# Optimization experiments

Hardware: AMD Instinct MI355X
Metric: run time of the kernel (lower is better)

Reference implementation:

```python
import jax, jax.numpy as jnp
import numpy as np
import math

# dims
B, T, HFEAT, E = 32, 8, 128, 128
NUM_CLS, NUM_GLOBAL = 4, 2
NSP = NUM_CLS + NUM_GLOBAL            # 6 special tokens
SCALES = (1, 4, 8)
WINDOW = 4
NHEAD = 8
DH = E // NHEAD                        # 16
NLAYERS = 2                            # blocks per scale = ceil(6/3)
NS = len(SCALES)
F = 512                                # dim_feedforward
ROPE_BASE = 100000.0
NEG = -1e9


def setup_inputs() -> dict:
    key = jax.random.key(0)
    ks = jax.random.split(key, 16)
    def rn(k, shape, s=0.02):
        return jax.random.normal(k, shape, jnp.float32) * s
    inp = {
        'embeddings': jax.random.normal(ks[0], (B, T, NSP + HFEAT, E), jnp.float32),
        'cls_tokens': rn(ks[1], (NUM_CLS, E)),
        'global_tokens': rn(ks[2], (NUM_GLOBAL, E)),
        'Wq': rn(ks[3], (NS, NLAYERS, E, E)),
        'bq': jnp.zeros((NS, NLAYERS, E), jnp.float32),
        'Wk': rn(ks[4], (NS, NLAYERS, E, E)),
        'bk': jnp.zeros((NS, NLAYERS, E), jnp.float32),
        'Wv': rn(ks[5], (NS, NLAYERS, E, E)),
        'bv': jnp.zeros((NS, NLAYERS, E), jnp.float32),
        'Wo': rn(ks[6], (NS, NLAYERS, E, E)),
        'bo': jnp.zeros((NS, NLAYERS, E), jnp.float32),
        'ln1_g': jnp.ones((NS, NLAYERS, E), jnp.float32),
        'ln1_b': jnp.zeros((NS, NLAYERS, E), jnp.float32),
        'ln2_g': jnp.ones((NS, NLAYERS, E), jnp.float32),
        'ln2_b': jnp.zeros((NS, NLAYERS, E), jnp.float32),
        'W1': rn(ks[7], (NS, NLAYERS, E, F)),
        'b1': jnp.zeros((NS, NLAYERS, F), jnp.float32),
        'W2': rn(ks[8], (NS, NLAYERS, F, E)),
        'b2': jnp.zeros((NS, NLAYERS, E), jnp.float32),
        'out_g': jnp.ones((E,), jnp.float32),
        'out_b': jnp.zeros((E,), jnp.float32),
    }
    return inp


def _layernorm(x, g, b, eps=1e-5):
    mu = x.mean(-1, keepdims=True)
    var = ((x - mu) ** 2).mean(-1, keepdims=True)
    return (x - mu) * jax.lax.rsqrt(var + eps) * g + b


def _rope(x):
    # x: (BT, L, H, DH); rotate-half RoPE over head dim
    L = x.shape[1]
    half = DH // 2
    inv = ROPE_BASE ** (-jnp.arange(half, dtype=jnp.float32) / half)
    ang = jnp.arange(L, dtype=jnp.float32)[:, None] * inv[None, :]   # (L, half)
    cos = jnp.cos(ang)[None, :, None, :]
    sin = jnp.sin(ang)[None, :, None, :]
    x1, x2 = x[..., :half], x[..., half:]
    return jnp.concatenate([x1 * cos - x2 * sin, x1 * sin + x2 * cos], axis=-1)


def _sparse_bias(L):
    # global(first NSP) rows/cols fully connected, others window +-WINDOW, diag allowed
    i = jnp.arange(L)
    allowed = (jnp.abs(i[:, None] - i[None, :]) <= WINDOW) | (i[:, None] < NSP) | (i[None, :] < NSP)
    return jnp.where(allowed, 0.0, NEG).astype(jnp.float32)  # (L, L) additive


def _encoder(x, s, Wq, bq, Wk, bk, Wv, bv, Wo, bo, ln1_g, ln1_b, ln2_g, ln2_b, W1, b1, W2, b2, bias):
    # x: (BT, L, E); pre-norm transformer encoder with RoPE attention
    BT, L, _ = x.shape
    for l in range(NLAYERS):
        h = _layernorm(x, ln1_g[s, l], ln1_b[s, l])
        q = (h @ Wq[s, l] + bq[s, l]).reshape(BT, L, NHEAD, DH)
        k = (h @ Wk[s, l] + bk[s, l]).reshape(BT, L, NHEAD, DH)
        v = (h @ Wv[s, l] + bv[s, l]).reshape(BT, L, NHEAD, DH)
        q, k = _rope(q), _rope(k)
        scores = jnp.einsum('blhd,bmhd->bhlm', q, k) / math.sqrt(DH) + bias[None, None]
        attn = jax.nn.softmax(scores, axis=-1)
        o = jnp.einsum('bhlm,bmhd->blhd', attn, v).reshape(BT, L, E)
        x = x + o @ Wo[s, l] + bo[s, l]
        h2 = _layernorm(x, ln2_g[s, l], ln2_b[s, l])
        x = x + jax.nn.gelu(h2 @ W1[s, l] + b1[s, l]) @ W2[s, l] + b2[s, l]
    return x


def reference(embeddings, cls_tokens, global_tokens, Wq, bq, Wk, bk, Wv, bv, Wo, bo,
              ln1_g, ln1_b, ln2_g, ln2_b, W1, b1, W2, b2, out_g, out_b):
    Bb, Tt, HC, Ee = embeddings.shape
    feats = embeddings[..., NSP:, :]                                 # (B,T,H,E)
    specials = jnp.broadcast_to(
        jnp.concatenate([cls_tokens, global_tokens], axis=0)[None, None],
        (Bb, Tt, NSP, Ee))
    cls_per_scale = []
    for s, g in enumerate(SCALES):
        H = feats.shape[2]
        K = H // g  # H divisible by all scales
        grouped = feats.reshape(Bb, Tt, K, g, Ee).mean(axis=3)       # contiguous mean grouping
        seq = jnp.concatenate([specials, grouped], axis=2)           # (B,T,L,E)
        L = NSP + K
        x = seq.reshape(Bb * Tt, L, Ee)
        bias = _sparse_bias(L)
        out = _encoder(x, s, Wq, bq, Wk, bk, Wv, bv, Wo, bo,
                       ln1_g, ln1_b, ln2_g, ln2_b, W1, b1, W2, b2, bias)
        cls_per_scale.append(out.reshape(Bb, Tt, L, Ee)[..., :NUM_CLS, :])
    cls_out = jnp.stack(cls_per_scale, axis=0).mean(axis=0)          # (B,T,num_cls,E)
    cls_out = _layernorm(cls_out, out_g, out_b)
    return cls_out.reshape(Bb, Tt, NUM_CLS * Ee)
```

## Files before the change

### kernel.cpp

```cpp
#include <hip/hip_runtime.h>
#include <hip/hip_bf16.h>

#define BT     256
#define EDIM   128
#define NSP    6
#define RT     49664
#define O1     34304
#define O2     44032
#define KSTR   20

typedef unsigned short u16;
typedef short s16x8 __attribute__((ext_vector_type(8)));
typedef float f32x4 __attribute__((ext_vector_type(4)));

__device__ __forceinline__ float u2f(u16 u){ union{unsigned i; float f;} v; v.i=((unsigned)u)<<16; return v.f; }
__device__ __forceinline__ u16 f2u(float f){
  union{float f; unsigned i;} v; v.f = f;
  unsigned r = v.i + 0x7FFF + ((v.i >> 16) & 1);
  return (u16)(r >> 16);
}
__device__ __forceinline__ float ldin(const void* p, size_t idx, int flag){
  return flag ? u2f(((const u16*)p)[idx]) : ((const float*)p)[idx];
}
__device__ __forceinline__ void unp8(uint4 v, float* f){
  f[0]=u2f((u16)(v.x)); f[1]=u2f((u16)(v.x>>16));
  f[2]=u2f((u16)(v.y)); f[3]=u2f((u16)(v.y>>16));
  f[4]=u2f((u16)(v.z)); f[5]=u2f((u16)(v.z>>16));
  f[6]=u2f((u16)(v.w)); f[7]=u2f((u16)(v.w>>16));
}

__device__ __forceinline__ void rowinfo(int row, int& s, int& r, int& L, int& g){
  if (row < O1){ s=0; r=row;    L=134; g=1; }
  else if (row < O2){ s=1; r=row-O1; L=38; g=4; }
  else { s=2; r=row-O2; L=22; g=8; }
}

__device__ __forceinline__ float gelu_f(float x){
  float t = tanhf(0.7978845608f*(x + 0.044715f*x*x*x));
  return 0.5f*x*(1.f+t);
}

__global__ void detect_k(const void* ln1g, int* flagp){
  unsigned v = *(const unsigned*)ln1g;
  *flagp = (v == 0x3F803F80u) ? 1 : 0;
}

struct CArg { const void* src; unsigned dstoff; unsigned n; unsigned inblk; unsigned outblk; };
struct CArgs { CArg a[12]; };
__global__ __launch_bounds__(256) void conv_k(CArgs ca, u16* stage, const int* flagp){
  int i = blockIdx.y;
  int flag = *flagp;
  const CArg& c = ca.a[i];
  for (unsigned idx = blockIdx.x*256u + threadIdx.x; idx < c.n; idx += gridDim.x*256u){
    unsigned blk = idx / c.inblk, r = idx % c.inblk;
    float v = flag ? u2f(((const u16*)c.src)[idx]) : ((const float*)c.src)[idx];
    stage[c.dstoff + blk*c.outblk + r] = flag ? ((const u16*)c.src)[idx] : f2u(v);
  }
}

__global__ __launch_bounds__(256) void convw_k(const void* s0, const void* s1, const void* s2,
                                               u16* dst, int K, int N, int Nsrc, const int* flagp)
{
  int flag = *flagp;
  const void* srcs[3] = {s0, s1, s2};
  int total = 6 * K * N;
  for (int idx = blockIdx.x*256 + threadIdx.x; idx < total; idx += gridDim.x*256) {
    int blk = idx / (K*N);
    int rem = idx % (K*N);
    int j = rem & 7;
    int t = rem >> 3;
    int n = t % N;
    int ck = t / N;
    int k = ck*8 + j;
    int w = n / Nsrc;
    int nn = n - w*Nsrc;
    size_t sidx = (size_t)blk*K*Nsrc + (size_t)k*Nsrc + nn;
    dst[idx] = flag ? ((const u16*)srcs[w])[sidx] : f2u(((const float*)srcs[w])[sidx]);
  }
}

__global__ __launch_bounds__(128) void build_k(const void* __restrict__ emb,
                                               const void* __restrict__ cls,
                                               const void* __restrict__ glob,
                                               float* __restrict__ x,
                                               u16* __restrict__ H,
                                               const u16* __restrict__ lnG,
                                               const u16* __restrict__ lnB,
                                               const int* flagp)
{
  __shared__ float red[4];
  int flag = *flagp;
  int row = blockIdx.x, e = threadIdx.x;
  int s, r, L, g; rowinfo(row, s, r, L, g);
  int seq = r / L, pos = r % L;
  float val;
  if (pos < NSP) {
    val = (pos < 4) ? ldin(cls, pos*EDIM + e, flag) : ldin(glob, (pos-4)*EDIM + e, flag);
  } else {
    int k = pos - NSP;
    size_t base = ((size_t)seq*134 + NSP + (size_t)k*g)*EDIM + e;
    float sum = 0.f;
    for (int j = 0; j < g; j++) sum += ldin(emb, base + (size_t)j*EDIM, flag);
    val = sum / (float)g;
  }
  x[(size_t)row*EDIM + e] = val;
  int wid = e >> 6;
  float sum = val, ss = val*val;
  #pragma unroll
  for (int off = 32; off; off >>= 1) { sum += __shfl_xor(sum, off); ss += __shfl_xor(ss, off); }
  if ((e & 63) == 0) { red[wid] = sum; red[2+wid] = ss; }
  __syncthreads();
  float ts = red[0]+red[1], tss = red[2]+red[3];
  float mu = ts * (1.f/128.f);
  float var = tss * (1.f/128.f) - mu*mu;
  float rs = rsqrtf(var + 1e-5f);
  const u16* gp = lnG + s*2*EDIM;
  const u16* bp = lnB + s*2*EDIM;
  H[(size_t)row*EDIM + e] = f2u((val-mu)*rs*u2f(gp[e]) + u2f(bp[e]));
}

template<int EPI, typename CT>
__global__ __launch_bounds__(256) void mgemm_k(
    const u16* __restrict__ A, int lda,
    const u16* __restrict__ Wt,
    const u16* __restrict__ Bias,
    CT* __restrict__ C, int ldc, int coff,
    int N, int K, int layer, int rowbase,
    u16* __restrict__ H, const u16* __restrict__ lnG, const u16* __restrict__ lnB, int lnidx)
{
  __shared__ u16 As[128*72];
  __shared__ u16 Bs[8*128*8];
  __shared__ float rsum[128][2];
  __shared__ float rss[128][2];
  const int row0 = blockIdx.x * 128;
  const int grow = rowbase + row0;
  const int n0 = blockIdx.y * 128;
  const int s = grow < O1 ? 0 : (grow < O2 ? 1 : 2);
  const u16* Wp = Wt + (size_t)(s*2+layer)*K*N;
  const u16* bp = Bias + (size_t)(s*2+layer)*N + n0;
  const int tid = threadIdx.x;
  const int lane = tid & 63, wave = tid >> 6;
  const int mw = (wave & 1) * 64, nw = (wave >> 1) * 64;
  const int g = lane >> 4, l15 = lane & 15;

  f32x4 acc[4][4];
  #pragma unroll
  for (int a = 0; a < 4; a++)
    #pragma unroll
    for (int b = 0; b < 4; b++) acc[a][b] = (f32x4){0.f,0.f,0.f,0.f};

  for (int k0 = 0; k0 < K; k0 += 64) {
    #pragma unroll
    for (int i = 0; i < 4; i++) {
      int unit = tid + i*256;
      int r = unit >> 3, kc = unit & 7;
      *(uint4*)&As[r*72 + kc*8] = *(const uint4*)(A + (size_t)(row0 + r)*lda + k0 + kc*8);
      int nn = unit & 127, kb = unit >> 7;
      *(uint4*)&Bs[(kb*128 + nn)*8] = *(const uint4*)(Wp + ((size_t)(k0/8 + kb)*N + n0 + nn)*8);
    }
    __syncthreads();
    #pragma unroll
    for (int ks = 0; ks < 2; ks++) {
      int c = ks*4 + g;
      s16x8 af[4], bfr[4];
      #pragma unroll
      for (int mt = 0; mt < 4; mt++) af[mt] = *(const s16x8*)&As[(mw + mt*16 + l15)*72 + c*8];
      #pragma unroll
      for (int nt = 0; nt < 4; nt++) bfr[nt] = *(const s16x8*)&Bs[(c*128 + nw + nt*16 + l15)*8];
      #pragma unroll
      for (int mt = 0; mt < 4; mt++)
        #pragma unroll
        for (int nt = 0; nt < 4; nt++)
          acc[mt][nt] = __builtin_amdgcn_mfma_f32_16x16x32_bf16(af[mt], bfr[nt], acc[mt][nt], 0, 0, 0);
    }
    __syncthreads();
  }
  float bb[4];
  #pragma unroll
  for (int nt = 0; nt < 4; nt++) bb[nt] = u2f(bp[nw + nt*16 + l15]);

  if (EPI == 3) {
    #pragma unroll
    for (int mt = 0; mt < 4; mt++) {
      #pragma unroll
      for (int reg = 0; reg < 4; reg++) {
        int row = row0 + mw + mt*16 + g*4 + reg;
        float ps = 0.f, pss = 0.f;
        #pragma unroll
        for (int nt = 0; nt < 4; nt++) {
          size_t cidx = (size_t)row*128 + nw + nt*16 + l15;
          float val = acc[mt][nt][reg] + bb[nt] + ((float*)C)[cidx];
          acc[mt][nt][reg] = val;
          ps += val; pss += val*val;
        }
        #pragma unroll
        for (int off = 1; off < 16; off <<= 1) {
          ps += __shfl_xor(ps, off); pss += __shfl_xor(pss, off);
        }
        if (l15 == 0) {
          int lr = mw + mt*16 + g*4 + reg;
          rsum[lr][nw>>6] = ps;
          rss[lr][nw>>6] = pss;
        }
      }
    }
    __syncthreads();
    const u16* gp = lnG + (s*2+lnidx)*EDIM;
    const u16* bpn = lnB + (s*2+lnidx)*EDIM;
    float gam[4], bet[4];
    #pragma unroll
    for (int nt = 0; nt < 4; nt++) { gam[nt] = u2f(gp[nw+nt*16+l15]); bet[nt] = u2f(bpn[nw+nt*16+l15]); }
    #pragma unroll
    for (int mt = 0; mt < 4; mt++) {
      #pragma unroll
      for (int reg = 0; reg < 4; reg++) {
        int lr = mw + mt*16 + g*4 + reg;
        int row = row0 + lr;
        float ts = rsum[lr][0]+rsum[lr][1], tss = rss[lr][0]+rss[lr][1];
        float mu = ts * (1.f/128.f);
        float var = tss * (1.f/128.f) - mu*mu;
        float rs = rsqrtf(var + 1e-5f);
        #pragma unroll
        for (int nt = 0; nt < 4; nt++) {
          size_t cidx = (size_t)row*128 + nw + nt*16 + l15;
          float val = acc[mt][nt][reg];
          ((float*)C)[cidx] = val;
          H[cidx] = f2u((val-mu)*rs*gam[nt] + bet[nt]);
        }
      }
    }
  } else {
    #pragma unroll
    for (int mt = 0; mt < 4; mt++) {
      #pragma unroll
      for (int reg = 0; reg < 4; reg++) {
        int row = row0 + mw + mt*16 + g*4 + reg;
        #pragma unroll
        for (int nt = 0; nt < 4; nt++) {
          float v = acc[mt][nt][reg] + bb[nt];
          size_t cidx = (size_t)row*ldc + coff + n0 + nw + nt*16 + l15;
          ((u16*)C)[cidx] = f2u(v);
        }
      }
    }
  }
}

template<int LNFUSE>
__global__ __launch_bounds__(256) void ffn_k(
    const u16* __restrict__ A,
    const u16* __restrict__ W1t, const u16* __restrict__ B1,
    const u16* __restrict__ W2t, const u16* __restrict__ B2,
    float* __restrict__ X,
    u16* __restrict__ H, const u16* __restrict__ lnG, const u16* __restrict__ lnB,
    int lnidx, int layer)
{
  __shared__ u16 As[64*136];
  __shared__ u16 Ts[64*72];
  __shared__ u16 Bs[8192];
  __shared__ float rsum[64][2];
  __shared__ float rss[64][2];
  const int row0 = blockIdx.x * 64;
  const int s = row0 < O1 ? 0 : (row0 < O2 ? 1 : 2);
  const u16* W1p = W1t + (size_t)(s*2+layer)*128*512;
  const u16* b1p = B1 + (s*2+layer)*512;
  const u16* W2p = W2t + (size_t)(s*2+layer)*512*128;
  const u16* b2p = B2 + (s*2+layer)*128;
  const int tid = threadIdx.x;
  const int lane = tid & 63, wave = tid >> 6;
  const int mw = (wave & 1) * 32;
  const int nw2 = (wave >> 1) * 32;
  const int nwC = (wave >> 1) * 64;
  const int g = lane >> 4, l15 = lane & 15;

  #pragma unroll
  for (int i = 0; i < 4; i++) {
    int unit = tid + i*256;
    int r = unit >> 4, kc = unit & 15;
    *(uint4*)&As[r*136 + kc*8] = *(const uint4*)(A + (size_t)(row0 + r)*128 + kc*8);
  }

  f32x4 acc2[2][4];
  #pragma unroll
  for (int a = 0; a < 2; a++)
    #pragma unroll
    for (int b = 0; b < 4; b++) acc2[a][b] = (f32x4){0.f,0.f,0.f,0.f};

  for (int f0 = 0; f0 < 512; f0 += 64) {
    __syncthreads();
    #pragma unroll
    for (int i = 0; i < 4; i++) {
      int unit = tid + i*256;
      int nn = unit & 63, kb = unit >> 6;
      *(uint4*)&Bs[(kb*64 + nn)*8] = *(const uint4*)(W1p + ((size_t)kb*512 + f0 + nn)*8);
    }
    __syncthreads();
    f32x4 acc1[2][2];
    #pragma unroll
    for (int a = 0; a < 2; a++)
      #pragma unroll
      for (int b = 0; b < 2; b++) acc1[a][b] = (f32x4){0.f,0.f,0.f,0.f};
    #pragma unroll
    for (int ks = 0; ks < 4; ks++) {
      int c = ks*4 + g;
      s16x8 af[2], bf[2];
      #pragma unroll
      for (int mt = 0; mt < 2; mt++) af[mt] = *(const s16x8*)&As[(mw + mt*16 + l15)*136 + c*8];
      #pragma unroll
      for (int nt = 0; nt < 2; nt++) bf[nt] = *(const s16x8*)&Bs[(c*64 + nw2 + nt*16 + l15)*8];
      #pragma unroll
      for (int mt = 0; mt < 2; mt++)
        #pragma unroll
        for (int nt = 0; nt < 2; nt++)
          acc1[mt][nt] = __builtin_amdgcn_mfma_f32_16x16x32_bf16(af[mt], bf[nt], acc1[mt][nt], 0, 0, 0);
    }
    #pragma unroll
    for (int nt = 0; nt < 2; nt++) {
      float bb1 = u2f(b1p[f0 + nw2 + nt*16 + l15]);
      #pragma unroll
      for (int mt = 0; mt < 2; mt++)
        #pragma unroll
        for (int reg = 0; reg < 4; reg++) {
          int row = mw + mt*16 + g*4 + reg;
          Ts[row*72 + nw2 + nt*16 + l15] = f2u(gelu_f(acc1[mt][nt][reg] + bb1));
        }
    }
    __syncthreads();
    #pragma unroll
    for (int i = 0; i < 4; i++) {
      int unit = tid + i*256;
      int nn = unit & 127, kb = unit >> 7;
      *(uint4*)&Bs[(kb*128 + nn)*8] = *(const uint4*)(W2p + ((size_t)(f0/8 + kb)*128 + nn)*8);
    }
    __syncthreads();
    #pragma unroll
    for (int ks = 0; ks < 2; ks++) {
      int c = ks*4 + g;
      s16x8 af[2], bf[4];
      #pragma unroll
      for (int mt = 0; mt < 2; mt++) af[mt] = *(const s16x8*)&Ts[(mw + mt*16 + l15)*72 + c*8];
      #pragma unroll
      for (int nt = 0; nt < 4; nt++) bf[nt] = *(const s16x8*)&Bs[(c*128 + nwC + nt*16 + l15)*8];
      #pragma unroll
      for (int mt = 0; mt < 2; mt++)
        #pragma unroll
        for (int nt = 0; nt < 4; nt++)
          acc2[mt][nt] = __builtin_amdgcn_mfma_f32_16x16x32_bf16(af[mt], bf[nt], acc2[mt][nt], 0, 0, 0);
    }
  }

  float bb2[4];
  #pragma unroll
  for (int nt = 0; nt < 4; nt++) bb2[nt] = u2f(b2p[nwC + nt*16 + l15]);

  if (LNFUSE) {
    #pragma unroll
    for (int mt = 0; mt < 2; mt++) {
      #pragma unroll
      for (int reg = 0; reg < 4; reg++) {
        int lr = mw + mt*16 + g*4 + reg;
        int row = row0 + lr;
        float ps = 0.f, pss = 0.f;
        #pragma unroll
        for (int nt = 0; nt < 4; nt++) {
          size_t cidx = (size_t)row*128 + nwC + nt*16 + l15;
          float val = acc2[mt][nt][reg] + bb2[nt] + X[cidx];
          acc2[mt][nt][reg] = val;
          ps += val; pss += val*val;
        }
        #pragma unroll
        for (int off = 1; off < 16; off <<= 1) {
          ps += __shfl_xor(ps, off); pss += __shfl_xor(pss, off);
        }
        if (l15 == 0) { rsum[lr][nwC>>6] = ps; rss[lr][nwC>>6] = pss; }
      }
    }
    __syncthreads();
    const u16* gp = lnG + (s*2+lnidx)*EDIM;
    const u16* bpn = lnB + (s*2+lnidx)*EDIM;
    float gam[4], bet[4];
    #pragma unroll
    for (int nt = 0; nt < 4; nt++) { gam[nt] = u2f(gp[nwC+nt*16+l15]); bet[nt] = u2f(bpn[nwC+nt*16+l15]); }
    #pragma unroll
    for (int mt = 0; mt < 2; mt++) {
      #pragma unroll
      for (int reg = 0; reg < 4; reg++) {
        int lr = mw + mt*16 + g*4 + reg;
        int row = row0 + lr;
        float ts = rsum[lr][0]+rsum[lr][1], tss = rss[lr][0]+rss[lr][1];
        float mu = ts * (1.f/128.f);
        float var = tss * (1.f/128.f) - mu*mu;
        float rs = rsqrtf(var + 1e-5f);
        #pragma unroll
        for (int nt = 0; nt < 4; nt++) {
          size_t cidx = (size_t)row*128 + nwC + nt*16 + l15;
          float val = acc2[mt][nt][reg];
          X[cidx] = val;
          H[cidx] = f2u((val-mu)*rs*gam[nt] + bet[nt]);
        }
      }
    }
  } else {
    #pragma unroll
    for (int mt = 0; mt < 2; mt++) {
      #pragma unroll
      for (int reg = 0; reg < 4; reg++) {
        int row = row0 + mw + mt*16 + g*4 + reg;
        #pragma unroll
        for (int nt = 0; nt < 4; nt++) {
          size_t cidx = (size_t)row*128 + nwC + nt*16 + l15;
          X[cidx] += acc2[mt][nt][reg] + bb2[nt];
        }
      }
    }
  }
}

__global__ __launch_bounds__(128) void attn_k(const u16* __restrict__ qkv, u16* __restrict__ o)
{
  __shared__ float Ks[134*KSTR];
  __shared__ float Vs[134*KSTR];
  int gseq = blockIdx.x, hd = blockIdx.y;
  int L, base;
  if (gseq < 256)      { L = 134; base = gseq*134; }
  else if (gseq < 512) { L = 38;  base = O1 + (gseq-256)*38; }
  else                 { L = 22;  base = O2 + (gseq-512)*22; }
  int tid = threadIdx.x;
  for (int u = tid; u < L*2; u += 128) {
    int kv = u & 1, row = u >> 1;
    const u16* p = qkv + (size_t)(base+row)*384 + 128 + kv*128 + hd*16;
    uint4 w0 = *(const uint4*)p, w1 = *(const uint4*)(p+8);
    float f[16];
    unp8(w0, f); unp8(w1, f+8);
    if (kv == 0) {
      #pragma unroll
      for (int d = 0; d < 8; d++) {
        float inv = __expf(-(float)d * (11.512925465f/8.f));
        float ang = (float)row * inv;
        float cs = __cosf(ang), sn = __sinf(ang);
        float a = f[d], b = f[d+8];
        f[d]   = a*cs - b*sn;
        f[d+8] = a*sn + b*cs;
      }
    }
    float* dst = (kv ? Vs : Ks) + row*KSTR;
    #pragma unroll
    for (int d = 0; d < 16; d++) dst[d] = f[d];
  }
  __syncthreads();

  for (int it = tid; it < L - NSP; it += 128) {
    int row = NSP + it;
    const u16* qp = qkv + (size_t)(base+row)*384 + hd*16;
    uint4 w0 = *(const uint4*)qp, w1 = *(const uint4*)(qp+8);
    float q[16]; unp8(w0, q); unp8(w1, q+8);
    #pragma unroll
    for (int d = 0; d < 8; d++) {
      float inv = __expf(-(float)d * (11.512925465f/8.f));
      float ang = (float)row * inv;
      float cs = __cosf(ang), sn = __sinf(ang);
      float a = q[d], b = q[d+8];
      q[d]   = a*cs - b*sn;
      q[d+8] = a*sn + b*cs;
    }
    float m = -1e30f, l = 0.f, oa[16] = {};
    auto step = [&](int j){
      const float4* kr = (const float4*)(Ks + j*KSTR);
      float4 k0 = kr[0], k1 = kr[1], k2 = kr[2], k3 = kr[3];
      float sc = q[0]*k0.x + q[1]*k0.y + q[2]*k0.z + q[3]*k0.w
               + q[4]*k1.x + q[5]*k1.y + q[6]*k1.z + q[7]*k1.w
               + q[8]*k2.x + q[9]*k2.y + q[10]*k2.z + q[11]*k2.w
               + q[12]*k3.x + q[13]*k3.y + q[14]*k3.z + q[15]*k3.w;
      sc *= 0.25f;
      float nm = fmaxf(m, sc);
      float scale = __expf(m - nm);
      float pexp = __expf(sc - nm);
      l = l*scale + pexp;
      const float4* vr = (const float4*)(Vs + j*KSTR);
      float4 v0 = vr[0], v1 = vr[1], v2 = vr[2], v3 = vr[3];
      oa[0]=oa[0]*scale+pexp*v0.x;  oa[1]=oa[1]*scale+pexp*v0.y;
      oa[2]=oa[2]*scale+pexp*v0.z;  oa[3]=oa[3]*scale+pexp*v0.w;
      oa[4]=oa[4]*scale+pexp*v1.x;  oa[5]=oa[5]*scale+pexp*v1.y;
      oa[6]=oa[6]*scale+pexp*v1.z;  oa[7]=oa[7]*scale+pexp*v1.w;
      oa[8]=oa[8]*scale+pexp*v2.x;  oa[9]=oa[9]*scale+pexp*v2.y;
      oa[10]=oa[10]*scale+pexp*v2.z; oa[11]=oa[11]*scale+pexp*v2.w;
      oa[12]=oa[12]*scale+pexp*v3.x; oa[13]=oa[13]*scale+pexp*v3.y;
      oa[14]=oa[14]*scale+pexp*v3.z; oa[15]=oa[15]*scale+pexp*v3.w;
      m = nm;
    };
    #pragma unroll
    for (int j = 0; j < NSP; j++) step(j);
    int jlo = (row-4 > NSP) ? row-4 : NSP;
    int jhi = (row+4 < L-1) ? row+4 : L-1;
    for (int j = jlo; j <= jhi; j++) step(j);
    float invl = 1.f/l;
    u16* op = o + (size_t)(base+row)*EDIM + hd*16;
    #pragma unroll
    for (int d = 0; d < 16; d++) op[d] = f2u(oa[d]*invl);
  }

  if (tid < 96) {
    int row = tid >> 4;
    int u = tid & 15;
    const u16* qp = qkv + (size_t)(base+row)*384 + hd*16;
    uint4 w0 = *(const uint4*)qp, w1 = *(const uint4*)(qp+8);
    float q[16]; unp8(w0, q); unp8(w1, q+8);
    #pragma unroll
    for (int d = 0; d < 8; d++) {
      float inv = __expf(-(float)d * (11.512925465f/8.f));
      float ang = (float)row * inv;
      float cs = __cosf(ang), sn = __sinf(ang);
      float a = q[d], b = q[d+8];
      q[d]   = a*cs - b*sn;
      q[d+8] = a*sn + b*cs;
    }
    float m = -1e30f, l = 0.f, oa[16] = {};
    for (int j = u; j < L; j += 16) {
      const float4* kr = (const float4*)(Ks + j*KSTR);
      float4 k0 = kr[0], k1 = kr[1], k2 = kr[2], k3 = kr[3];
      float sc = q[0]*k0.x + q[1]*k0.y + q[2]*k0.z + q[3]*k0.w
               + q[4]*k1.x + q[5]*k1.y + q[6]*k1.z + q[7]*k1.w
               + q[8]*k2.x + q[9]*k2.y + q[10]*k2.z + q[11]*k2.w
               + q[12]*k3.x + q[13]*k3.y + q[14]*k3.z + q[15]*k3.w;
      sc *= 0.25f;
      float nm = fmaxf(m, sc);
      float scale = __expf(m - nm);
      float pexp = __expf(sc - nm);
      l = l*scale + pexp;
      const float4* vr = (const float4*)(Vs + j*KSTR);
      float4 v0 = vr[0], v1 = vr[1], v2 = vr[2], v3 = vr[3];
      oa[0]=oa[0]*scale+pexp*v0.x;  oa[1]=oa[1]*scale+pexp*v0.y;
      oa[2]=oa[2]*scale+pexp*v0.z;  oa[3]=oa[3]*scale+pexp*v0.w;
      oa[4]=oa[4]*scale+pexp*v1.x;  oa[5]=oa[5]*scale+pexp*v1.y;
      oa[6]=oa[6]*scale+pexp*v1.z;  oa[7]=oa[7]*scale+pexp*v1.w;
      oa[8]=oa[8]*scale+pexp*v2.x;  oa[9]=oa[9]*scale+pexp*v2.y;
      oa[10]=oa[10]*scale+pexp*v2.z; oa[11]=oa[11]*scale+pexp*v2.w;
      oa[12]=oa[12]*scale+pexp*v3.x; oa[13]=oa[13]*scale+pexp*v3.y;
      oa[14]=oa[14]*scale+pexp*v3.z; oa[15]=oa[15]*scale+pexp*v3.w;
      m = nm;
    }
    #pragma unroll
    for (int off = 1; off < 16; off <<= 1) {
      float m2 = __shfl_xor(m, off);
      float l2 = __shfl_xor(l, off);
      float nm = fmaxf(m, m2);
      float s1 = __expf(m - nm), s2 = __expf(m2 - nm);
      #pragma unroll
      for (int d = 0; d < 16; d++) {
        float o2 = __shfl_xor(oa[d], off);
        oa[d] = oa[d]*s1 + o2*s2;
      }
      l = l*s1 + l2*s2;
      m = nm;
    }
    if (u == 0) {
      float invl = 1.f/l;
      u16* op = o + (size_t)(base+row)*EDIM + hd*16;
      #pragma unroll
      for (int d = 0; d < 16; d++) op[d] = f2u(oa[d]*invl);
    }
  }
}

__global__ __launch_bounds__(256) void final_k(const float* __restrict__ x,
                                               const u16* __restrict__ G,
                                               const u16* __restrict__ Bt,
                                               void* __restrict__ out, const int* flagp)
{
  int flag = *flagp;
  int wid = threadIdx.x >> 6, lane = threadIdx.x & 63;
  int idx = blockIdx.x*4 + wid;
  int seq = idx >> 2, c = idx & 3;
  size_t r0 = ((size_t)seq*134 + c)*EDIM;
  size_t r1 = ((size_t)O1 + (size_t)seq*38 + c)*EDIM;
  size_t r2 = ((size_t)O2 + (size_t)seq*22 + c)*EDIM;
  float v0 = (x[r0+lane]    + x[r1+lane]    + x[r2+lane])    * (1.f/3.f);
  float v1 = (x[r0+64+lane] + x[r1+64+lane] + x[r2+64+lane]) * (1.f/3.f);
  float sum = v0 + v1;
  #pragma unroll
  for (int off = 32; off; off >>= 1) sum += __shfl_xor(sum, off);
  float mu = sum * (1.f/128.f);
  float d0 = v0 - mu, d1 = v1 - mu;
  float var = d0*d0 + d1*d1;
  #pragma unroll
  for (int off = 32; off; off >>= 1) var += __shfl_xor(var, off);
  var *= (1.f/128.f);
  float rs = rsqrtf(var + 1e-5f);
  float o0 = d0*rs*u2f(G[lane])    + u2f(Bt[lane]);
  float o1 = d1*rs*u2f(G[64+lane]) + u2f(Bt[64+lane]);
  size_t oi0 = (size_t)seq*512 + c*128 + lane;
  if (flag) { ((u16*)out)[oi0] = f2u(o0); ((u16*)out)[oi0+64] = f2u(o1); }
  else      { ((float*)out)[oi0] = o0;    ((float*)out)[oi0+64] = o1; }
}

#define S_WQKV 0u
#define S_BQKV 294912u
#define S_WO   297216u
#define S_BO   395520u
#define S_W1   396288u
#define S_B1   789504u
#define S_W2   792576u
#define S_B2   1185792u
#define S_L1G  1186560u
#define S_L1B  1187328u
#define S_L2G  1188096u
#define S_L2B  1188864u
#define S_OG   1189632u
#define S_OB   1189760u

extern "C" void kernel_launch(void* const* d_in, const int* in_sizes, int n_in,
                              void* d_out, int out_size, void* d_ws, size_t ws_size,
                              hipStream_t stream) {
  char* wsb = (char*)d_ws;
  int*   flagp = (int*)wsb;
  u16*   stage = (u16*)(wsb + 64);
  float* x     = (float*)(wsb + (size_t)2379840);
  u16*   h     = (u16*)(wsb + (size_t)27807808);
  u16*   qkv   = (u16*)(wsb + (size_t)40521792);

  detect_k<<<1, 1, 0, stream>>>(d_in[11], flagp);

  CArgs ca;
  CArg list[12] = {
    { d_in[4],  S_BQKV,       768, 128, 384 },
    { d_in[6],  S_BQKV+128u,  768, 128, 384 },
    { d_in[8],  S_BQKV+256u,  768, 128, 384 },
    { d_in[10], S_BO,         768, 128, 128 },
    { d_in[16], S_B1,        3072, 512, 512 },
    { d_in[18], S_B2,         768, 128, 128 },
    { d_in[11], S_L1G,        768, 128, 128 },
    { d_in[12], S_L1B,        768, 128, 128 },
    { d_in[13], S_L2G,        768, 128, 128 },
    { d_in[14], S_L2B,        768, 128, 128 },
    { d_in[19], S_OG,         128, 128, 128 },
    { d_in[20], S_OB,         128, 128, 128 },
  };
  for (int i = 0; i < 12; i++) ca.a[i] = list[i];
  conv_k<<<dim3(4, 12), 256, 0, stream>>>(ca, stage, flagp);

  convw_k<<<256, 256, 0, stream>>>(d_in[3], d_in[5], d_in[7], stage+S_WQKV, 128, 384, 128, flagp);
  convw_k<<<128, 256, 0, stream>>>(d_in[9], d_in[9], d_in[9], stage+S_WO,   128, 128, 128, flagp);
  convw_k<<<256, 256, 0, stream>>>(d_in[15],d_in[15],d_in[15],stage+S_W1,   128, 512, 512, flagp);
  convw_k<<<256, 256, 0, stream>>>(d_in[17],d_in[17],d_in[17],stage+S_W2,   512, 128, 128, flagp);

  build_k<<<RT, 128, 0, stream>>>(d_in[0], d_in[1], d_in[2], x, h, stage+S_L1G, stage+S_L1B, flagp);

  for (int l = 0; l < 2; l++) {
    mgemm_k<0, u16><<<dim3(RT/128, 3), 256, 0, stream>>>(h, 128, stage+S_WQKV, stage+S_BQKV, qkv, 384, 0, 384, 128, l, 0, nullptr, nullptr, nullptr, 0);
    attn_k<<<dim3(768, 8), 128, 0, stream>>>(qkv, h);
    mgemm_k<3, float><<<dim3(RT/128, 1), 256, 0, stream>>>(h, 128, stage+S_WO, stage+S_BO, x, 128, 0, 128, 128, l, 0, h, stage+S_L2G, stage+S_L2B, l);
    if (l == 0)
      ffn_k<1><<<RT/64, 256, 0, stream>>>(h, stage+S_W1, stage+S_B1, stage+S_W2, stage+S_B2, x, h, stage+S_L1G, stage+S_L1B, 1, l);
    else
      ffn_k<0><<<RT/64, 256, 0, stream>>>(h, stage+S_W1, stage+S_B1, stage+S_W2, stage+S_B2, x, nullptr, nullptr, nullptr, 0, l);
  }
  final_k<<<BT, 256, 0, stream>>>(x, stage+S_OG, stage+S_OB, d_out, flagp);
}
```

Before: 414.3 us.

## Replace 128-row QKV/out-proj GEMM with 64-row full-K tile and per-wave LN epilogue

Replaces the 128x128-tile GEMM that looped over K with a 64-row tile that loads all of K=128 at once. Each wave now owns 16 full rows, so the residual+LayerNorm epilogue reduces with shuffles only, with no shared-memory cross-wave reduction. It also merges the four weight-conversion launches into one 2D launch and rewrites GELU's tanh as an exp-based sigmoid form. The trade-off is more blocks and weight reloads per row, plus a slightly different GELU numeric path.

Result: slower. 438.7 us (+5.9%).

```diff
diff --git a/kernel.cpp b/kernel.cpp
--- a/kernel.cpp
+++ b/kernel.cpp
@@ -36,8 +36,10 @@
 }
 
 __device__ __forceinline__ float gelu_f(float x){
-  float t = tanhf(0.7978845608f*(x + 0.044715f*x*x*x));
-  return 0.5f*x*(1.f+t);
+  float u = 1.5957691216f*(x + 0.044715f*x*x*x);
+  u = fminf(u, 80.f);
+  float w = __expf(u);
+  return x * w / (w + 1.f);
 }
 
 __global__ void detect_k(const void* ln1g, int* flagp){
@@ -58,23 +60,26 @@
   }
 }
 
-__global__ __launch_bounds__(256) void convw_k(const void* s0, const void* s1, const void* s2,
-                                               u16* dst, int K, int N, int Nsrc, const int* flagp)
+struct WArg { const void* s0; const void* s1; const void* s2; unsigned off; int K; int N; int Nsrc; };
+struct WArgs { WArg a[4]; };
+__global__ __launch_bounds__(256) void convw_k(WArgs wa, u16* stage, const int* flagp)
 {
   int flag = *flagp;
-  const void* srcs[3] = {s0, s1, s2};
-  int total = 6 * K * N;
+  const WArg& a = wa.a[blockIdx.y];
+  const void* srcs[3] = {a.s0, a.s1, a.s2};
+  int total = 6 * a.K * a.N;
+  u16* dst = stage + a.off;
   for (int idx = blockIdx.x*256 + threadIdx.x; idx < total; idx += gridDim.x*256) {
-    int blk = idx / (K*N);
-    int rem = idx % (K*N);
+    int blk = idx / (a.K*a.N);
+    int rem = idx % (a.K*a.N);
     int j = rem & 7;
     int t = rem >> 3;
-    int n = t % N;
-    int ck = t / N;
+    int n = t % a.N;
+    int ck = t / a.N;
     int k = ck*8 + j;
-    int w = n / Nsrc;
-    int nn = n - w*Nsrc;
-    size_t sidx = (size_t)blk*K*Nsrc + (size_t)k*Nsrc + nn;
+    int w = n / a.Nsrc;
+    int nn = n - w*a.Nsrc;
+    size_t sidx = (size_t)blk*a.K*a.Nsrc + (size_t)k*a.Nsrc + nn;
     dst[idx] = flag ? ((const u16*)srcs[w])[sidx] : f2u(((const float*)srcs[w])[sidx]);
   }
 }
@@ -119,128 +124,91 @@
   H[(size_t)row*EDIM + e] = f2u((val-mu)*rs*u2f(gp[e]) + u2f(bp[e]));
 }
 
-template<int EPI, typename CT>
-__global__ __launch_bounds__(256) void mgemm_k(
-    const u16* __restrict__ A, int lda,
-    const u16* __restrict__ Wt,
-    const u16* __restrict__ Bias,
-    CT* __restrict__ C, int ldc, int coff,
-    int N, int K, int layer, int rowbase,
-    u16* __restrict__ H, const u16* __restrict__ lnG, const u16* __restrict__ lnB, int lnidx)
+template<int EPI>
+__global__ __launch_bounds__(256) void gemm64_k(
+    const u16* __restrict__ A,
+    const u16* __restrict__ Wt, const u16* __restrict__ Bias,
+    u16* __restrict__ C, int ldc, int N, int layer,
+    float* __restrict__ X, u16* __restrict__ H,
+    const u16* __restrict__ lnG, const u16* __restrict__ lnB, int lnidx)
 {
-  __shared__ u16 As[128*72];
-  __shared__ u16 Bs[8*128*8];
-  __shared__ float rsum[128][2];
-  __shared__ float rss[128][2];
-  const int row0 = blockIdx.x * 128;
-  const int grow = rowbase + row0;
+  __shared__ u16 As[4][16*136];
+  __shared__ u16 Bs[16*128*8];
+  const int row0 = blockIdx.x * 64;
   const int n0 = blockIdx.y * 128;
-  const int s = grow < O1 ? 0 : (grow < O2 ? 1 : 2);
-  const u16* Wp = Wt + (size_t)(s*2+layer)*K*N;
+  const int s = row0 < O1 ? 0 : (row0 < O2 ? 1 : 2);
+  const u16* Wp = Wt + (size_t)(s*2+layer)*128*N;
   const u16* bp = Bias + (size_t)(s*2+layer)*N + n0;
   const int tid = threadIdx.x;
-  const int lane = tid & 63, wave = tid >> 6;
-  const int mw = (wave & 1) * 64, nw = (wave >> 1) * 64;
+  const int lane = tid & 63, w = tid >> 6;
   const int g = lane >> 4, l15 = lane & 15;
 
-  f32x4 acc[4][4];
-  #pragma unroll
-  for (int a = 0; a < 4; a++)
-    #pragma unroll
-    for (int b = 0; b < 4; b++) acc[a][b] = (f32x4){0.f,0.f,0.f,0.f};
-
-  for (int k0 = 0; k0 < K; k0 += 64) {
-    #pragma unroll
-    for (int i = 0; i < 4; i++) {
-      int unit = tid + i*256;
-      int r = unit >> 3, kc = unit & 7;
-      *(uint4*)&As[r*72 + kc*8] = *(const uint4*)(A + (size_t)(row0 + r)*lda + k0 + kc*8);
-      int nn = unit & 127, kb = unit >> 7;
-      *(uint4*)&Bs[(kb*128 + nn)*8] = *(const uint4*)(Wp + ((size_t)(k0/8 + kb)*N + n0 + nn)*8);
-    }
-    __syncthreads();
-    #pragma unroll
-    for (int ks = 0; ks < 2; ks++) {
-      int c = ks*4 + g;
-      s16x8 af[4], bfr[4];
-      #pragma unroll
-      for (int mt = 0; mt < 4; mt++) af[mt] = *(const s16x8*)&As[(mw + mt*16 + l15)*72 + c*8];
-      #pragma unroll
-      for (int nt = 0; nt < 4; nt++) bfr[nt] = *(const s16x8*)&Bs[(c*128 + nw + nt*16 + l15)*8];
-      #pragma unroll
-      for (int mt = 0; mt < 4; mt++)
-        #pragma unroll
-        for (int nt = 0; nt < 4; nt++)
-          acc[mt][nt] = __builtin_amdgcn_mfma_f32_16x16x32_bf16(af[mt], bfr[nt], acc[mt][nt], 0, 0, 0);
-    }
-    __syncthreads();
-  }
-  float bb[4];
-  #pragma unroll
-  for (int nt = 0; nt < 4; nt++) bb[nt] = u2f(bp[nw + nt*16 + l15]);
-
-  if (EPI == 3) {
-    #pragma unroll
-    for (int mt = 0; mt < 4; mt++) {
-      #pragma unroll
-      for (int reg = 0; reg < 4; reg++) {
-        int row = row0 + mw + mt*16 + g*4 + reg;
-        float ps = 0.f, pss = 0.f;
-        #pragma unroll
-        for (int nt = 0; nt < 4; nt++) {
-          size_t cidx = (size_t)row*128 + nw + nt*16 + l15;
-          float val = acc[mt][nt][reg] + bb[nt] + ((float*)C)[cidx];
-          acc[mt][nt][reg] = val;
-          ps += val; pss += val*val;
-        }
-        #pragma unroll
-        for (int off = 1; off < 16; off <<= 1) {
-          ps += __shfl_xor(ps, off); pss += __shfl_xor(pss, off);
-        }
-        if (l15 == 0) {
-          int lr = mw + mt*16 + g*4 + reg;
-          rsum[lr][nw>>6] = ps;
-          rss[lr][nw>>6] = pss;
-        }
-      }
-    }
-    __syncthreads();
+  #pragma unroll
+  for (int i = 0; i < 4; i++) {
+    int unit = lane + i*64;
+    int r = unit >> 4, kc = unit & 15;
+    *(uint4*)&As[w][r*136 + kc*8] = *(const uint4*)(A + (size_t)(row0 + w*16 + r)*128 + kc*8);
+  }
+  #pragma unroll
+  for (int i = 0; i < 8; i++) {
+    int u = tid + i*256;
+    int kb = u >> 7, nn = u & 127;
+    *(uint4*)&Bs[u*8] = *(const uint4*)(Wp + ((size_t)kb*N + n0 + nn)*8);
+  }
+  __syncthreads();
+
+  f32x4 acc[8];
+  #pragma unroll
+  for (int nt = 0; nt < 8; nt++) acc[nt] = (f32x4){0.f,0.f,0.f,0.f};
+  #pragma unroll
+  for (int ks = 0; ks < 4; ks++) {
+    int c = ks*4 + g;
+    s16x8 af = *(const s16x8*)&As[w][l15*136 + c*8];
+    #pragma unroll
+    for (int nt = 0; nt < 8; nt++) {
+      s16x8 bf = *(const s16x8*)&Bs[(c*128 + nt*16 + l15)*8];
+      acc[nt] = __builtin_amdgcn_mfma_f32_16x16x32_bf16(af, bf, acc[nt], 0, 0, 0);
+    }
+  }
+
+  float bb[8];
+  #pragma unroll
+  for (int nt = 0; nt < 8; nt++) bb[nt] = u2f(bp[nt*16 + l15]);
+
+  if (EPI == 0) {
+    #pragma unroll
+    for (int reg = 0; reg < 4; reg++) {
+      int row = row0 + w*16 + g*4 + reg;
+      #pragma unroll
+      for (int nt = 0; nt < 8; nt++)
+        C[(size_t)row*ldc + n0 + nt*16 + l15] = f2u(acc[nt][reg] + bb[nt]);
+    }
+  } else {
+    float gam[8], bet[8];
     const u16* gp = lnG + (s*2+lnidx)*EDIM;
     const u16* bpn = lnB + (s*2+lnidx)*EDIM;
-    float gam[4], bet[4];
-    #pragma unroll
-    for (int nt = 0; nt < 4; nt++) { gam[nt] = u2f(gp[nw+nt*16+l15]); bet[nt] = u2f(bpn[nw+nt*16+l15]); }
-    #pragma unroll
-    for (int mt = 0; mt < 4; mt++) {
-      #pragma unroll
-      for (int reg = 0; reg < 4; reg++) {
-        int lr = mw + mt*16 + g*4 + reg;
-        int row = row0 + lr;
-        float ts = rsum[lr][0]+rsum[lr][1], tss = rss[lr][0]+rss[lr][1];
-        float mu = ts * (1.f/128.f);
-        float var = tss * (1.f/128.f) - mu*mu;
-        float rs = rsqrtf(var + 1e-5f);
-        #pragma unroll
-        for (int nt = 0; nt < 4; nt++) {
-          size_t cidx = (size_t)row*128 + nw + nt*16 + l15;
-          float val = acc[mt][nt][reg];
-          ((float*)C)[cidx] = val;
-          H[cidx] = f2u((val-mu)*rs*gam[nt] + bet[nt]);
-        }
+    #pragma unroll
+    for (int nt = 0; nt < 8; nt++) { gam[nt] = u2f(gp[nt*16+l15]); bet[nt] = u2f(bpn[nt*16+l15]); }
+    #pragma unroll
+    for (int reg = 0; reg < 4; reg++) {
+      int row = row0 + w*16 + g*4 + reg;
+      float vals[8], ps = 0.f, pss = 0.f;
+      #pragma unroll
+      for (int nt = 0; nt < 8; nt++) {
+        size_t cidx = (size_t)row*128 + nt*16 + l15;
+        float v = acc[nt][reg] + bb[nt] + X[cidx];
+        vals[nt] = v; ps += v; pss += v*v;
       }
-    }
-  } else {
-    #pragma unroll
-    for (int mt = 0; mt < 4; mt++) {
-      #pragma unroll
-      for (int reg = 0; reg < 4; reg++) {
-        int row = row0 + mw + mt*16 + g*4 + reg;
-        #pragma unroll
-        for (int nt = 0; nt < 4; nt++) {
-          float v = acc[mt][nt][reg] + bb[nt];
-          size_t cidx = (size_t)row*ldc + coff + n0 + nw + nt*16 + l15;
-          ((u16*)C)[cidx] = f2u(v);
-        }
+      #pragma unroll
+      for (int off = 1; off < 16; off <<= 1) { ps += __shfl_xor(ps, off); pss += __shfl_xor(pss, off); }
+      float mu = ps * (1.f/128.f);
+      float var = pss * (1.f/128.f) - mu*mu;
+      float rs = rsqrtf(var + 1e-5f);
+      #pragma unroll
+      for (int nt = 0; nt < 8; nt++) {
+        size_t cidx = (size_t)row*128 + nt*16 + l15;
+        X[cidx] = vals[nt];
+        H[cidx] = f2u((vals[nt]-mu)*rs*gam[nt] + bet[nt]);
       }
     }
   }
@@ -638,17 +606,21 @@
   for (int i = 0; i < 12; i++) ca.a[i] = list[i];
   conv_k<<<dim3(4, 12), 256, 0, stream>>>(ca, stage, flagp);
 
-  convw_k<<<256, 256, 0, stream>>>(d_in[3], d_in[5], d_in[7], stage+S_WQKV, 128, 384, 128, flagp);
-  convw_k<<<128, 256, 0, stream>>>(d_in[9], d_in[9], d_in[9], stage+S_WO,   128, 128, 128, flagp);
-  convw_k<<<256, 256, 0, stream>>>(d_in[15],d_in[15],d_in[15],stage+S_W1,   128, 512, 512, flagp);
-  convw_k<<<256, 256, 0, stream>>>(d_in[17],d_in[17],d_in[17],stage+S_W2,   512, 128, 128, flagp);
+  WArgs wa;
+  wa.a[0] = { d_in[3],  d_in[5],  d_in[7],  S_WQKV, 128, 384, 128 };
+  wa.a[1] = { d_in[9],  d_in[9],  d_in[9],  S_WO,   128, 128, 128 };
+  wa.a[2] = { d_in[15], d_in[15], d_in[15], S_W1,   128, 512, 512 };
+  wa.a[3] = { d_in[17], d_in[17], d_in[17], S_W2,   512, 128, 128 };
+  convw_k<<<dim3(192, 4), 256, 0, stream>>>(wa, stage, flagp);
 
   build_k<<<RT, 128, 0, stream>>>(d_in[0], d_in[1], d_in[2], x, h, stage+S_L1G, stage+S_L1B, flagp);
 
   for (int l = 0; l < 2; l++) {
-    mgemm_k<0, u16><<<dim3(RT/128, 3), 256, 0, stream>>>(h, 128, stage+S_WQKV, stage+S_BQKV, qkv, 384, 0, 384, 128, l, 0, nullptr, nullptr, nullptr, 0);
+    gemm64_k<0><<<dim3(RT/64, 3), 256, 0, stream>>>(h, stage+S_WQKV, stage+S_BQKV, qkv, 384, 384, l,
+                                                    nullptr, nullptr, nullptr, nullptr, 0);
     attn_k<<<dim3(768, 8), 128, 0, stream>>>(qkv, h);
-    mgemm_k<3, float><<<dim3(RT/128, 1), 256, 0, stream>>>(h, 128, stage+S_WO, stage+S_BO, x, 128, 0, 128, 128, l, 0, h, stage+S_L2G, stage+S_L2B, l);
+    gemm64_k<3><<<dim3(RT/64, 1), 256, 0, stream>>>(h, stage+S_WO, stage+S_BO, nullptr, 128, 128, l,
+                                                    x, h, stage+S_L2G, stage+S_L2B, l);
     if (l == 0)
       ffn_k<1><<<RT/64, 256, 0, stream>>>(h, stage+S_W1, stage+S_B1, stage+S_W2, stage+S_B2, x, h, stage+S_L1G, stage+S_L1B, 1, l);
     else
```
